# Kernel tuning notes

Hardware: AMD Instinct MI355X
Metric: run time of the kernel (lower is better)

The kernel has to match this reference:

```python
import math
import jax, jax.numpy as jnp
import numpy as np

_INIT_LOG_GAIN = math.log(5.0)
B, L, D = 4, 1024, 256


def setup_inputs() -> dict:
    key = jax.random.key(0)
    kq, kk = jax.random.split(key)
    q = jax.random.normal(kq, (B, L, D), dtype=jnp.float32)
    k = jax.random.normal(kk, (B, L, D), dtype=jnp.float32)
    P_prev = jnp.zeros((B, D, D), dtype=jnp.float32)
    log_gain = jnp.full((D,), _INIT_LOG_GAIN, dtype=jnp.float32)
    output_scale = jnp.ones((D,), dtype=jnp.float32)
    return {"q": q, "k": k, "P_prev": P_prev, "log_gain": log_gain,
            "output_scale": output_scale}


def reference(q, k, P_prev, log_gain, output_scale):
    """Sequential rank-1 projection-state update + normalized matvec + gated tanh.

    q, k: [B, L, D]; P_prev: [B, D, D]. Returns (q_out [B,L,D], P_final [B,D,D]).
    """
    gain = jnp.exp(log_gain)  # effective gain, [D]

    def step(P, qk_t):
        q_t, k_t = qk_t                                   # each [B, D]
        P = P + jnp.einsum('bi,bj->bij', k_t, k_t)        # rank-1 update
        fro = jnp.sqrt(jnp.sum(P * P, axis=(-2, -1), keepdims=True))
        P_norm = P / (fro + 1e-7)
        q_aligned = jnp.einsum('bij,bj->bi', P_norm, q_t)
        q_safe = jnp.tanh(gain * q_aligned) * output_scale
        return P, q_safe

    # scan over the L time axis
    P_final, outs = jax.lax.scan(step, P_prev,
                                 (jnp.swapaxes(q, 0, 1), jnp.swapaxes(k, 0, 1)))
    q_out = jnp.swapaxes(outs, 0, 1)  # [B, L, D]
    return q_out, P_final
```

## Files before the change

### kernel.cpp

```cpp
#include <hip/hip_runtime.h>
#include <math.h>


#define LDSPAD 68

typedef __attribute__((ext_vector_type(8))) short bf16x8;
typedef __attribute__((ext_vector_type(4))) float f32x4;

__device__ __forceinline__ unsigned short f2bf(float x) {
    union { float f; unsigned u; } c; c.f = x;
    return (unsigned short)((c.u + (0x7fffu + ((c.u >> 16) & 1u))) >> 16);
}
__device__ __forceinline__ unsigned f2bf2(float a, float b) {
    union { float f; unsigned u; } ca, cb; ca.f = a; cb.f = b;
    unsigned ua = ca.u + (0x7fffu + ((ca.u >> 16) & 1u));
    unsigned ub = cb.u + (0x7fffu + ((cb.u >> 16) & 1u));
    return (ua >> 16) | (ub & 0xffff0000u);
}
__device__ __forceinline__ void gload16(const void* g, const void* l) {
    __builtin_amdgcn_global_load_lds(
        (const __attribute__((address_space(1))) unsigned int*)g,
        (__attribute__((address_space(3))) unsigned int*)l, 16, 0, 0);
}
__device__ __forceinline__ bf16x8 ldsfrag(const unsigned short* lds, int row0, int g0, int lane) {
    int r = row0 + (lane & 15);
    int g = g0 + (lane >> 4);
    return *(const bf16x8*)(lds + r * 64 + (((g ^ (r & 7)) & 7) << 3));
}
__device__ __forceinline__ bf16x8 ldsfragf32(const char* tile, int row0, int lane) {
    int r = row0 + (lane & 15);
    int g0 = (lane >> 4) << 1;
    float4 a = *(const float4*)(tile + r * 128 + (((g0 ^ (r & 7)) & 7) << 4));
    float4 b = *(const float4*)(tile + r * 128 + ((((g0 + 1) ^ (r & 7)) & 7) << 4));
    union { unsigned u[4]; bf16x8 v; } o;
    o.u[0] = f2bf2(a.x, a.y); o.u[1] = f2bf2(a.z, a.w);
    o.u[2] = f2bf2(b.x, b.y); o.u[3] = f2bf2(b.z, b.w);
    return o.v;
}
#define MFMA16(a, b, c) __builtin_amdgcn_mfma_f32_16x16x32_bf16(a, b, c, 0, 0, 0)

__global__ __launch_bounds__(256) void k_gsp(
    const float* __restrict__ Q, const float* __restrict__ K,
    const float* __restrict__ Pprev,
    unsigned short* __restrict__ Sc, float* __restrict__ r2d, float* __restrict__ P4,
    unsigned short* __restrict__ KT, float* __restrict__ basePart,
    int B_, int L, int D, int nT, int nPairs)
{
    __shared__ char smem[49152];
    int tid = threadIdx.x, lane = tid & 63, w = tid >> 6;
    int fr = lane & 15, fq = lane >> 4;
    int nDt = D >> 6, nLt = L >> 6;
    int nGS = B_ * nPairs;
    int nP4 = B_ * nDt * nDt * 4;
    int nKT = B_ * nLt * nDt;
    int bx = blockIdx.x;
    int id = (bx < nGS) ? ((bx & 7) * (nGS >> 3) + (bx >> 3)) : bx;

    if (id < nGS) {
        int p = id % nPairs;
        int b = id / nPairs;
        int ti = (int)((sqrtf(8.f * p + 1.f) - 1.f) * 0.5f);
        while ((ti + 1) * (ti + 2) / 2 <= p) ti++;
        while (ti * (ti + 1) / 2 > p) ti--;
        int sj = p - ti * (ti + 1) / 2;

        const float* Qf = Q + (size_t)b * L * D;
        const float* Kf = K + (size_t)b * L * D;
        int t0 = ti * 64, s0 = sj * 64;
        int wr = w >> 1, wc = w & 1;

        f32x4 g00 = {0,0,0,0}, g01 = {0,0,0,0}, g10 = {0,0,0,0}, g11 = {0,0,0,0};
        f32x4 s00 = {0,0,0,0}, s01 = {0,0,0,0}, s10 = {0,0,0,0}, s11 = {0,0,0,0};

        auto STAGE = [&](int ck, int bo) {
            const float* Kt = Kf + (size_t)t0 * D + ck * 32;
            const float* Qt = Qf + (size_t)t0 * D + ck * 32;
            const float* Ks = Kf + (size_t)s0 * D + ck * 32;
            for (int c = w; c < 8; c += 4) {
                int lrow = c * 8 + (lane >> 3);
                int gof = lrow * D + ((((lane & 7) ^ (lrow & 7)) & 7) << 2);
                gload16(Kt + gof, smem + bo + c * 1024);
                gload16(Qt + gof, smem + bo + 8192 + c * 1024);
                gload16(Ks + gof, smem + bo + 16384 + c * 1024);
            }
        };

        STAGE(0, 0);
        __syncthreads();
        for (int ck = 0; ck < 8; ck++) {
            int cur = (ck & 1) * 24576;
            if (ck < 7) STAGE(ck + 1, 24576 - cur);
            const char* Kt = smem + cur;
            const char* Qt = Kt + 8192;
            const char* Ks = Kt + 16384;
            bf16x8 bK0 = ldsfragf32(Ks, wc * 32, lane);
            bf16x8 bK1 = ldsfragf32(Ks, wc * 32 + 16, lane);
            bf16x8 aK0 = ldsfragf32(Kt, wr * 32, lane);
            bf16x8 aK1 = ldsfragf32(Kt, wr * 32 + 16, lane);
            bf16x8 aQ0 = ldsfragf32(Qt, wr * 32, lane);
            bf16x8 aQ1 = ldsfragf32(Qt, wr * 32 + 16, lane);
            g00 = MFMA16(aK0, bK0, g00);
            g01 = MFMA16(aK0, bK1, g01);
            g10 = MFMA16(aK1, bK0, g10);
            g11 = MFMA16(aK1, bK1, g11);
            s00 = MFMA16(aQ0, bK0, s00);
            s01 = MFMA16(aQ0, bK1, s01);
            s10 = MFMA16(aQ1, bK0, s10);
            s11 = MFMA16(aQ1, bK1, s11);
            __syncthreads();
        }

        float rsv[2][4] = {{0, 0, 0, 0}, {0, 0, 0, 0}};
        unsigned short* sb = (unsigned short*)smem;
#define EPI(MI, NI, AG, AS) { _Pragma("unroll") \
        for (int reg = 0; reg < 4; reg++) { \
            int tl = wr * 32 + MI * 16 + fq * 4 + reg; \
            int sl2 = wc * 32 + NI * 16 + fr; \
            int t = ti * 64 + tl, s = sj * 64 + sl2; \
            float g = AG[reg]; \
            float wgt = (s < t) ? 2.f : (s == t ? 1.f : 0.f); \
            rsv[MI][reg] += wgt * g * g; \
            sb[tl * 64 + sl2] = f2bf((s <= t) ? AS[reg] : 0.f); \
        } }
        EPI(0, 0, g00, s00) EPI(0, 1, g01, s01)
        EPI(1, 0, g10, s10) EPI(1, 1, g11, s11)
#undef EPI
        __syncthreads();
        {
            unsigned short* ScT = Sc + ((size_t)(b * nPairs + p) << 12);
            const uint4* s4 = (const uint4*)sb;
            uint4* d4 = (uint4*)ScT;
            d4[tid] = s4[tid];
            d4[tid + 256] = s4[tid + 256];
        }
#pragma unroll
        for (int off = 1; off < 16; off <<= 1) {
#pragma unroll
            for (int mi = 0; mi < 2; mi++)
#pragma unroll
                for (int reg = 0; reg < 4; reg++)
                    rsv[mi][reg] += __shfl_xor(rsv[mi][reg], off);
        }
        if (fr == 0) {
#pragma unroll
            for (int mi = 0; mi < 2; mi++)
#pragma unroll
                for (int reg = 0; reg < 4; reg++) {
                    int t = ti * 64 + wr * 32 + mi * 16 + fq * 4 + reg;
                    r2d[((size_t)(b * 2 * nT) + sj * 2 + wc) * L + t] = rsv[mi][reg];
                }
        }
    } else if (id < nGS + nP4) {
        int id2 = id - nGS;
        int nIJ = nDt * nDt;
        int lc = id2 & 3;
        int ij = (id2 >> 2) % nIJ;
        int b = id2 / (4 * nIJ);
        int ib = (ij / nDt) * 64, jb = (ij % nDt) * 64;
        int tchunk = L >> 2;
        int tstart = lc * tchunk;
        const float* Kf = K + (size_t)b * L * D;
        float* lA = (float*)smem;
        float* lB = lA + 32 * LDSPAD;
        int tx = tid & 15, ty = tid >> 4;
        float acc[4][4] = {};
        for (int tc = 0; tc < tchunk; tc += 32) {
            __syncthreads();
            for (int f = tid; f < 512; f += 256) {
                int r = f >> 4, c4 = (f & 15) * 4;
                *(float4*)&lA[r * LDSPAD + c4] =
                    *(const float4*)(Kf + (size_t)(tstart + tc + r) * D + ib + c4);
                *(float4*)&lB[r * LDSPAD + c4] =
                    *(const float4*)(Kf + (size_t)(tstart + tc + r) * D + jb + c4);
            }
            __syncthreads();
#pragma unroll 8
            for (int t2 = 0; t2 < 32; t2++) {
                float4 av = *(const float4*)&lA[t2 * LDSPAD + ty * 4];
                float4 bv = *(const float4*)&lB[t2 * LDSPAD + tx * 4];
                float aa[4] = {av.x, av.y, av.z, av.w};
                float ba[4] = {bv.x, bv.y, bv.z, bv.w};
#pragma unroll
                for (int i = 0; i < 4; i++)
#pragma unroll
                    for (int j = 0; j < 4; j++) acc[i][j] += aa[i] * ba[j];
            }
        }
        float* dst = P4 + ((((size_t)b * nIJ + ij) * 4 + lc) * 4096);
#pragma unroll
        for (int i = 0; i < 4; i++) {
            float4 o = {acc[i][0], acc[i][1], acc[i][2], acc[i][3]};
            *(float4*)(dst + (ty * 4 + i) * 64 + tx * 4) = o;
        }
    } else if (id < nGS + nP4 + nKT) {
        int id2 = id - nGS - nP4;
        int dt = id2 % nDt, lt = (id2 / nDt) % nLt, b = id2 / (nDt * nLt);
        int l0 = lt * 64, d0 = dt * 64;
        const float* Kf = K + (size_t)b * L * D;
        unsigned short* KTp = KT + (size_t)b * D * L;
        float* lds = (float*)smem;
        int r = tid >> 2, cq = (tid & 3) << 4;
#pragma unroll
        for (int i = 0; i < 16; i += 4) {
            float4 kv = *(const float4*)(Kf + (size_t)(l0 + r) * D + d0 + cq + i);
            lds[r * 65 + cq + i] = kv.x;     lds[r * 65 + cq + i + 1] = kv.y;
            lds[r * 65 + cq + i + 2] = kv.z; lds[r * 65 + cq + i + 3] = kv.w;
        }
        __syncthreads();
        int d2 = tid >> 2, cl = (tid & 3) << 4;
#pragma unroll
        for (int i = 0; i < 16; i += 2) {
            *(unsigned*)(KTp + (size_t)(d0 + d2) * L + l0 + cl + i) =
                f2bf2(lds[(cl + i) * 65 + d2], lds[(cl + i + 1) * 65 + d2]);
        }
    } else {
        int id2 = id - nGS - nP4 - nKT;
        int n = D * D / 16;
        const float* P = Pprev + (size_t)(id2 >> 4) * D * D + (size_t)(id2 & 15) * n;
        float* lds = (float*)smem;
        float s = 0.f;
        for (int i = tid * 4; i < n; i += 1024) {
            float4 vv = *(const float4*)(P + i);
            s += vv.x * vv.x + vv.y * vv.y + vv.z * vv.z + vv.w * vv.w;
        }
#pragma unroll
        for (int off = 32; off; off >>= 1) s += __shfl_down(s, off);
        if (lane == 0) lds[w] = s;
        __syncthreads();
        if (tid == 0) basePart[id2] = lds[0] + lds[1] + lds[2] + lds[3];
    }
}

__global__ __launch_bounds__(256) void k_yp(
    const float* __restrict__ Q, const float* __restrict__ K,
    const float* __restrict__ Pprev, const float* __restrict__ log_gain,
    const float* __restrict__ oscale,
    const unsigned short* __restrict__ Sc, const float* __restrict__ r2d,
    const unsigned short* __restrict__ KT, const float* __restrict__ basePart,
    const float* __restrict__ P4,
    float* __restrict__ out, float* __restrict__ outP,
    int B_, int L, int D, int nT, int nPairs)
{
    __shared__ unsigned short ys[18432];
    __shared__ float invf[1024];
    __shared__ float wred[4];
    int tid = threadIdx.x, lane = tid & 63, w = tid >> 6;
    int fr = lane & 15, fq = lane >> 4;
    int nDt = D >> 6;
    int nDh = 16;
    int nY = B_ * (nT >> 1) * nDh;
    int bx = blockIdx.x;
    int id = (bx < nY) ? ((bx & 7) * (nY >> 3) + (bx >> 3)) : bx;

    if (id < nY) {
        int dh = id % nDh;
        int u = (id / nDh) % (nT >> 1);
        int b = id / (nDh * (nT >> 1));
        int d0 = dh * 16;

        float bb = 0.f;
#pragma unroll
        for (int i = 0; i < 16; i++) bb += basePart[b * 16 + i];

        int t0v = tid * 4;
        int ns = 2 * ((t0v >> 6) + 1);
        float4 vs = {0.f, 0.f, 0.f, 0.f};
        for (int j = 0; j < ns; j++) {
            float4 rr = *(const float4*)&r2d[((size_t)(b * 2 * nT) + j) * L + t0v];
            vs.x += rr.x; vs.y += rr.y; vs.z += rr.z; vs.w += rr.w;
        }
        float v[4] = {vs.x, vs.y, vs.z, vs.w};
        if (bb != 0.f) {
#pragma unroll
            for (int u2 = 0; u2 < 4; u2++) {
                int t = t0v + u2;
                const float* kt = K + ((size_t)b * L + t) * D;
                const float* P = Pprev + (size_t)b * D * D;
                float c = 0.f;
                for (int i = 0; i < D; i++) {
                    float a2 = 0.f;
                    for (int j2 = 0; j2 < D; j2++) a2 += P[i * D + j2] * kt[j2];
                    c += kt[i] * a2;
                }
                v[u2] += 2.f * c;
            }
        }
        v[1] += v[0]; v[2] += v[1]; v[3] += v[2];
        float tot = v[3], sc2 = tot;
        for (int off = 1; off < 64; off <<= 1) {
            float n2 = __shfl_up(sc2, off);
            if (lane >= off) sc2 += n2;
        }
        if (lane == 63) wred[w] = sc2;
        __syncthreads();
        float woff = 0.f;
        for (int i2 = 0; i2 < w; i2++) woff += wred[i2];
        float exc = woff + sc2 - tot;
#pragma unroll
        for (int u2 = 0; u2 < 4; u2++)
            invf[t0v + u2] = 1.f / (sqrtf(bb + exc + v[u2]) + 1e-7f);
        __syncthreads();

        int twl = w << 4;
        int ti0 = u, ti1 = nT - 1 - u;
        int pb0 = ti0 * (ti0 + 1) / 2, pb1 = ti1 * (ti1 + 1) / 2;
        const unsigned short* ScB = Sc + ((size_t)b * nPairs << 12);
        const unsigned short* KTb = KT + (size_t)b * D * L;

        f32x4 c0 = {0, 0, 0, 0};
        f32x4 c1 = {0, 0, 0, 0};

        auto STAGE = [&](int sj, int bo) {
            const unsigned short* T1p = ScB + ((size_t)(pb1 + sj) << 12);
            if (sj <= u) {
                const unsigned short* T0p = ScB + ((size_t)(pb0 + sj) << 12);
                for (int c = w; c < 8; c += 4) {
                    int lrow = c * 8 + (lane >> 3);
                    int go = lrow * 64 + ((((lane & 7) ^ (lrow & 7)) & 7) << 3);
                    gload16(T0p + go, ys + bo + c * 512);
                }
            }
            for (int c = w; c < 8; c += 4) {
                int lrow = c * 8 + (lane >> 3);
                int go = lrow * 64 + ((((lane & 7) ^ (lrow & 7)) & 7) << 3);
                gload16(T1p + go, ys + bo + 4096 + c * 512);
            }
            if (w < 2) {
                int lrow = w * 8 + (lane >> 3);
                int gsw = (((lane & 7) ^ (lrow & 7)) & 7) << 3;
                gload16(KTb + (size_t)(d0 + lrow) * L + sj * 64 + gsw,
                        ys + bo + 8192 + w * 512);
            }
        };

        STAGE(0, 0);
        __syncthreads();
        for (int sj = 0; sj <= ti1; sj++) {
            int cur = (sj & 1) * 9216;
            if (sj < ti1) STAGE(sj + 1, 9216 - cur);
            const unsigned short* S0 = ys + cur;
            const unsigned short* S1 = S0 + 4096;
            const unsigned short* KTl = S0 + 8192;
#pragma unroll
            for (int kc = 0; kc < 2; kc++) {
                bf16x8 b0 = ldsfrag(KTl, 0, kc * 4, lane);
                bf16x8 A1 = ldsfrag(S1, twl, kc * 4, lane);
                c1 = MFMA16(A1, b0, c1);
                if (sj <= ti0) {
                    bf16x8 A0 = ldsfrag(S0, twl, kc * 4, lane);
                    c0 = MFMA16(A0, b0, c0);
                }
            }
            __syncthreads();
        }

        if (bb != 0.f) {
            const float* Qf = Q + (size_t)b * L * D;
            const float* Pb = Pprev + (size_t)b * D * D;
            for (int jj = 0; jj < D; jj++) {
                float p0 = Pb[(size_t)(d0 + fr) * D + jj];
#pragma unroll
                for (int reg = 0; reg < 4; reg++) {
                    float q0v = Qf[(size_t)(ti0 * 64 + twl + fq * 4 + reg) * D + jj];
                    float q1v = Qf[(size_t)(ti1 * 64 + twl + fq * 4 + reg) * D + jj];
                    c0[reg] += q0v * p0;
                    c1[reg] += q1v * p0;
                }
            }
        }

        float gg0 = expf(log_gain[d0 + fr]), os0 = oscale[d0 + fr];
        float* outb = out + (size_t)b * L * D;
#pragma unroll
        for (int reg = 0; reg < 4; reg++) {
            int t0 = ti0 * 64 + twl + fq * 4 + reg;
            int t1 = ti1 * 64 + twl + fq * 4 + reg;
            outb[(size_t)t0 * D + d0 + fr] = tanhf(gg0 * c0[reg] * invf[t0]) * os0;
            outb[(size_t)t1 * D + d0 + fr] = tanhf(gg0 * c1[reg] * invf[t1]) * os0;
        }
    } else {
        int id2 = id - nY;
        int nIJ = nDt * nDt;
        size_t e = ((size_t)id2 * 256 + tid) * 8;
        int b = (int)(e / ((size_t)D * D));
        int rem = (int)(e % ((size_t)D * D));
        int i = rem / D, j = rem % D;
        int ij = (i >> 6) * nDt + (j >> 6);
        int li = i & 63, lj = j & 63;
        const float* src = P4 + ((size_t)b * nIJ + ij) * 4 * 4096 + li * 64 + lj;
        float4 o0 = *(const float4*)(Pprev + e);
        float4 o1 = *(const float4*)(Pprev + e + 4);
#pragma unroll
        for (int lc = 0; lc < 4; lc++) {
            float4 a0 = *(const float4*)(src + lc * 4096);
            float4 a1 = *(const float4*)(src + lc * 4096 + 4);
            o0.x += a0.x; o0.y += a0.y; o0.z += a0.z; o0.w += a0.w;
            o1.x += a1.x; o1.y += a1.y; o1.z += a1.z; o1.w += a1.w;
        }
        *(float4*)(outP + e) = o0;
        *(float4*)(outP + e + 4) = o1;
    }
}

extern "C" void kernel_launch(void* const* d_in, const int* in_sizes, int n_in,
                              void* d_out, int out_size, void* d_ws, size_t ws_size,
                              hipStream_t stream) {
    const float* q = (const float*)d_in[0];
    const float* k = (const float*)d_in[1];
    const float* Pprev = (const float*)d_in[2];
    const float* log_gain = (const float*)d_in[3];
    const float* oscale = (const float*)d_in[4];

    int D = in_sizes[3];
    int B = in_sizes[2] / (D * D);
    int L = in_sizes[0] / (B * D);
    int nT = L / 64;
    int nPairs = nT * (nT + 1) / 2;
    int nDt = D >> 6;
    int nLt = L >> 6;
    int nIJ = nDt * nDt;

    if (D != 256 || L != 1024) return;

    float* out = (float*)d_out;
    float* outP = out + (size_t)B * L * D;

    size_t sR = (size_t)B * L * 2 * nT;
    size_t sBP = 64;
    size_t sP4 = (size_t)B * nIJ * 4 * 4096;
    size_t sSc = (size_t)B * nPairs * 4096;
    size_t sKT = (size_t)B * D * L;
    size_t need = (sR + sBP + sP4) * sizeof(float) + (sSc + sKT) * 2;
    if (ws_size < need) return;

    float* r2d = (float*)d_ws;
    float* basePart = r2d + sR;
    float* P4 = basePart + sBP;
    unsigned short* Sc = (unsigned short*)(P4 + sP4);
    unsigned short* KT = Sc + sSc;

    int grid1 = B * nPairs + B * nIJ * 4 + B * nLt * nDt + B * 16;
    int grid2 = B * (nT >> 1) * 16 + (B * D * D) / 2048;

    k_gsp<<<grid1, 256, 0, stream>>>(q, k, Pprev, Sc, r2d, P4, KT, basePart,
                                     B, L, D, nT, nPairs);
    k_yp<<<grid2, 256, 0, stream>>>(q, k, Pprev, log_gain, oscale, Sc, r2d, KT,
                                    basePart, P4, out, outP, B, L, D, nT, nPairs);
}
```

Before: 56.62 us.

## Compute final P via split-bf16 MFMA and hoist per-batch norm scan to own kernel

The final-state rank-update K^T K, previously done with FP32 scalar FMA into four partial buffers and reduced in the second kernel, is now computed in the second kernel with bf16 MFMA using a hi/lo split of K (three products) for near-fp32 accuracy. The first kernel writes both high and low bf16 transposed K. The cumulative Frobenius-norm prefix scan, previously recomputed by every output block, moves into a small separate per-batch kernel that writes inverse norms. This trades an extra launch and the hi/lo storage traffic for less redundant work and tensor-core use.

```diff
diff --git a/kernel.cpp b/kernel.cpp
--- a/kernel.cpp
+++ b/kernel.cpp
@@ -1,8 +1,6 @@
 #include <hip/hip_runtime.h>
 #include <math.h>
 
-
-#define LDSPAD 68
 
 typedef __attribute__((ext_vector_type(8))) short bf16x8;
 typedef __attribute__((ext_vector_type(4))) float f32x4;
@@ -16,6 +14,9 @@
     unsigned ua = ca.u + (0x7fffu + ((ca.u >> 16) & 1u));
     unsigned ub = cb.u + (0x7fffu + ((cb.u >> 16) & 1u));
     return (ua >> 16) | (ub & 0xffff0000u);
+}
+__device__ __forceinline__ float bf2f(unsigned short h) {
+    union { unsigned u; float f; } c; c.u = ((unsigned)h) << 16; return c.f;
 }
 __device__ __forceinline__ void gload16(const void* g, const void* l) {
     __builtin_amdgcn_global_load_lds(
@@ -42,8 +43,9 @@
 __global__ __launch_bounds__(256) void k_gsp(
     const float* __restrict__ Q, const float* __restrict__ K,
     const float* __restrict__ Pprev,
-    unsigned short* __restrict__ Sc, float* __restrict__ r2d, float* __restrict__ P4,
-    unsigned short* __restrict__ KT, float* __restrict__ basePart,
+    unsigned short* __restrict__ Sc, float* __restrict__ r2d,
+    unsigned short* __restrict__ KThi, unsigned short* __restrict__ KTlo,
+    float* __restrict__ basePart,
     int B_, int L, int D, int nT, int nPairs)
 {
     __shared__ char smem[49152];
@@ -51,7 +53,6 @@
     int fr = lane & 15, fq = lane >> 4;
     int nDt = D >> 6, nLt = L >> 6;
     int nGS = B_ * nPairs;
-    int nP4 = B_ * nDt * nDt * 4;
     int nKT = B_ * nLt * nDt;
     int bx = blockIdx.x;
     int id = (bx < nGS) ? ((bx & 7) * (nGS >> 3) + (bx >> 3)) : bx;
@@ -150,54 +151,13 @@
                     r2d[((size_t)(b * 2 * nT) + sj * 2 + wc) * L + t] = rsv[mi][reg];
                 }
         }
-    } else if (id < nGS + nP4) {
+    } else if (id < nGS + nKT) {
         int id2 = id - nGS;
-        int nIJ = nDt * nDt;
-        int lc = id2 & 3;
-        int ij = (id2 >> 2) % nIJ;
-        int b = id2 / (4 * nIJ);
-        int ib = (ij / nDt) * 64, jb = (ij % nDt) * 64;
-        int tchunk = L >> 2;
-        int tstart = lc * tchunk;
-        const float* Kf = K + (size_t)b * L * D;
-        float* lA = (float*)smem;
-        float* lB = lA + 32 * LDSPAD;
-        int tx = tid & 15, ty = tid >> 4;
-        float acc[4][4] = {};
-        for (int tc = 0; tc < tchunk; tc += 32) {
-            __syncthreads();
-            for (int f = tid; f < 512; f += 256) {
-                int r = f >> 4, c4 = (f & 15) * 4;
-                *(float4*)&lA[r * LDSPAD + c4] =
-                    *(const float4*)(Kf + (size_t)(tstart + tc + r) * D + ib + c4);
-                *(float4*)&lB[r * LDSPAD + c4] =
-                    *(const float4*)(Kf + (size_t)(tstart + tc + r) * D + jb + c4);
-            }
-            __syncthreads();
-#pragma unroll 8
-            for (int t2 = 0; t2 < 32; t2++) {
-                float4 av = *(const float4*)&lA[t2 * LDSPAD + ty * 4];
-                float4 bv = *(const float4*)&lB[t2 * LDSPAD + tx * 4];
-                float aa[4] = {av.x, av.y, av.z, av.w};
-                float ba[4] = {bv.x, bv.y, bv.z, bv.w};
-#pragma unroll
-                for (int i = 0; i < 4; i++)
-#pragma unroll
-                    for (int j = 0; j < 4; j++) acc[i][j] += aa[i] * ba[j];
-            }
-        }
-        float* dst = P4 + ((((size_t)b * nIJ + ij) * 4 + lc) * 4096);
-#pragma unroll
-        for (int i = 0; i < 4; i++) {
-            float4 o = {acc[i][0], acc[i][1], acc[i][2], acc[i][3]};
-            *(float4*)(dst + (ty * 4 + i) * 64 + tx * 4) = o;
-        }
-    } else if (id < nGS + nP4 + nKT) {
-        int id2 = id - nGS - nP4;
         int dt = id2 % nDt, lt = (id2 / nDt) % nLt, b = id2 / (nDt * nLt);
         int l0 = lt * 64, d0 = dt * 64;
         const float* Kf = K + (size_t)b * L * D;
-        unsigned short* KTp = KT + (size_t)b * D * L;
+        unsigned short* KThp = KThi + (size_t)b * D * L;
+        unsigned short* KTlp = KTlo + (size_t)b * D * L;
         float* lds = (float*)smem;
         int r = tid >> 2, cq = (tid & 3) << 4;
 #pragma unroll
@@ -210,11 +170,15 @@
         int d2 = tid >> 2, cl = (tid & 3) << 4;
 #pragma unroll
         for (int i = 0; i < 16; i += 2) {
-            *(unsigned*)(KTp + (size_t)(d0 + d2) * L + l0 + cl + i) =
-                f2bf2(lds[(cl + i) * 65 + d2], lds[(cl + i + 1) * 65 + d2]);
+            float v0 = lds[(cl + i) * 65 + d2];
+            float v1 = lds[(cl + i + 1) * 65 + d2];
+            unsigned short h0 = f2bf(v0), h1 = f2bf(v1);
+            size_t off = (size_t)(d0 + d2) * L + l0 + cl + i;
+            *(unsigned*)(KThp + off) = (unsigned)h0 | ((unsigned)h1 << 16);
+            *(unsigned*)(KTlp + off) = f2bf2(v0 - bf2f(h0), v1 - bf2f(h1));
         }
     } else {
-        int id2 = id - nGS - nP4 - nKT;
+        int id2 = id - nGS - nKT;
         int n = D * D / 16;
         const float* P = Pprev + (size_t)(id2 >> 4) * D * D + (size_t)(id2 & 15) * n;
         float* lds = (float*)smem;
@@ -231,22 +195,71 @@
     }
 }
 
+__global__ __launch_bounds__(256) void k_scan(
+    const float* __restrict__ K, const float* __restrict__ Pprev,
+    const float* __restrict__ r2d, const float* __restrict__ basePart,
+    float* __restrict__ invfro, int B_, int L, int D, int nT)
+{
+    __shared__ float wred[4];
+    int b = blockIdx.x;
+    int tid = threadIdx.x, lane = tid & 63, w = tid >> 6;
+    float bb = 0.f;
+#pragma unroll
+    for (int i = 0; i < 16; i++) bb += basePart[b * 16 + i];
+
+    int t0v = tid * 4;
+    int ns = 2 * ((t0v >> 6) + 1);
+    float4 vs = {0.f, 0.f, 0.f, 0.f};
+    for (int j = 0; j < ns; j++) {
+        float4 rr = *(const float4*)&r2d[((size_t)(b * 2 * nT) + j) * L + t0v];
+        vs.x += rr.x; vs.y += rr.y; vs.z += rr.z; vs.w += rr.w;
+    }
+    float v[4] = {vs.x, vs.y, vs.z, vs.w};
+    if (bb != 0.f) {
+#pragma unroll
+        for (int u2 = 0; u2 < 4; u2++) {
+            int t = t0v + u2;
+            const float* kt = K + ((size_t)b * L + t) * D;
+            const float* P = Pprev + (size_t)b * D * D;
+            float c = 0.f;
+            for (int i = 0; i < D; i++) {
+                float a2 = 0.f;
+                for (int j2 = 0; j2 < D; j2++) a2 += P[i * D + j2] * kt[j2];
+                c += kt[i] * a2;
+            }
+            v[u2] += 2.f * c;
+        }
+    }
+    v[1] += v[0]; v[2] += v[1]; v[3] += v[2];
+    float tot = v[3], sc2 = tot;
+    for (int off = 1; off < 64; off <<= 1) {
+        float n2 = __shfl_up(sc2, off);
+        if (lane >= off) sc2 += n2;
+    }
+    if (lane == 63) wred[w] = sc2;
+    __syncthreads();
+    float woff = 0.f;
+    for (int i2 = 0; i2 < w; i2++) woff += wred[i2];
+    float exc = woff + sc2 - tot;
+#pragma unroll
+    for (int u2 = 0; u2 < 4; u2++)
+        invfro[(size_t)b * L + t0v + u2] = 1.f / (sqrtf(bb + exc + v[u2]) + 1e-7f);
+}
+
 __global__ __launch_bounds__(256) void k_yp(
-    const float* __restrict__ Q, const float* __restrict__ K,
+    const float* __restrict__ Q,
     const float* __restrict__ Pprev, const float* __restrict__ log_gain,
     const float* __restrict__ oscale,
-    const unsigned short* __restrict__ Sc, const float* __restrict__ r2d,
-    const unsigned short* __restrict__ KT, const float* __restrict__ basePart,
-    const float* __restrict__ P4,
+    const unsigned short* __restrict__ Sc, const float* __restrict__ invfro,
+    const unsigned short* __restrict__ KThi, const unsigned short* __restrict__ KTlo,
+    const float* __restrict__ basePart,
     float* __restrict__ out, float* __restrict__ outP,
     int B_, int L, int D, int nT, int nPairs)
 {
     __shared__ unsigned short ys[18432];
     __shared__ float invf[1024];
-    __shared__ float wred[4];
     int tid = threadIdx.x, lane = tid & 63, w = tid >> 6;
     int fr = lane & 15, fq = lane >> 4;
-    int nDt = D >> 6;
     int nDh = 16;
     int nY = B_ * (nT >> 1) * nDh;
     int bx = blockIdx.x;
@@ -261,51 +274,14 @@
         float bb = 0.f;
 #pragma unroll
         for (int i = 0; i < 16; i++) bb += basePart[b * 16 + i];
-
-        int t0v = tid * 4;
-        int ns = 2 * ((t0v >> 6) + 1);
-        float4 vs = {0.f, 0.f, 0.f, 0.f};
-        for (int j = 0; j < ns; j++) {
-            float4 rr = *(const float4*)&r2d[((size_t)(b * 2 * nT) + j) * L + t0v];
-            vs.x += rr.x; vs.y += rr.y; vs.z += rr.z; vs.w += rr.w;
-        }
-        float v[4] = {vs.x, vs.y, vs.z, vs.w};
-        if (bb != 0.f) {
-#pragma unroll
-            for (int u2 = 0; u2 < 4; u2++) {
-                int t = t0v + u2;
-                const float* kt = K + ((size_t)b * L + t) * D;
-                const float* P = Pprev + (size_t)b * D * D;
-                float c = 0.f;
-                for (int i = 0; i < D; i++) {
-                    float a2 = 0.f;
-                    for (int j2 = 0; j2 < D; j2++) a2 += P[i * D + j2] * kt[j2];
-                    c += kt[i] * a2;
-                }
-                v[u2] += 2.f * c;
-            }
-        }
-        v[1] += v[0]; v[2] += v[1]; v[3] += v[2];
-        float tot = v[3], sc2 = tot;
-        for (int off = 1; off < 64; off <<= 1) {
-            float n2 = __shfl_up(sc2, off);
-            if (lane >= off) sc2 += n2;
-        }
-        if (lane == 63) wred[w] = sc2;
-        __syncthreads();
-        float woff = 0.f;
-        for (int i2 = 0; i2 < w; i2++) woff += wred[i2];
-        float exc = woff + sc2 - tot;
-#pragma unroll
-        for (int u2 = 0; u2 < 4; u2++)
-            invf[t0v + u2] = 1.f / (sqrtf(bb + exc + v[u2]) + 1e-7f);
+        *(float4*)&invf[tid * 4] = *(const float4*)&invfro[(size_t)b * L + tid * 4];
         __syncthreads();
 
         int twl = w << 4;
         int ti0 = u, ti1 = nT - 1 - u;
         int pb0 = ti0 * (ti0 + 1) / 2, pb1 = ti1 * (ti1 + 1) / 2;
         const unsigned short* ScB = Sc + ((size_t)b * nPairs << 12);
-        const unsigned short* KTb = KT + (size_t)b * D * L;
+        const unsigned short* KTb = KThi + (size_t)b * D * L;
 
         f32x4 c0 = {0, 0, 0, 0};
         f32x4 c1 = {0, 0, 0, 0};
@@ -380,25 +356,54 @@
         }
     } else {
         int id2 = id - nY;
-        int nIJ = nDt * nDt;
-        size_t e = ((size_t)id2 * 256 + tid) * 8;
-        int b = (int)(e / ((size_t)D * D));
-        int rem = (int)(e % ((size_t)D * D));
-        int i = rem / D, j = rem % D;
-        int ij = (i >> 6) * nDt + (j >> 6);
-        int li = i & 63, lj = j & 63;
-        const float* src = P4 + ((size_t)b * nIJ + ij) * 4 * 4096 + li * 64 + lj;
-        float4 o0 = *(const float4*)(Pprev + e);
-        float4 o1 = *(const float4*)(Pprev + e + 4);
-#pragma unroll
-        for (int lc = 0; lc < 4; lc++) {
-            float4 a0 = *(const float4*)(src + lc * 4096);
-            float4 a1 = *(const float4*)(src + lc * 4096 + 4);
-            o0.x += a0.x; o0.y += a0.y; o0.z += a0.z; o0.w += a0.w;
-            o1.x += a1.x; o1.y += a1.y; o1.z += a1.z; o1.w += a1.w;
-        }
-        *(float4*)(outP + e) = o0;
-        *(float4*)(outP + e + 4) = o1;
+        int b = id2 >> 4, ij = id2 & 15;
+        int i0 = (ij >> 2) << 6, j0 = (ij & 3) << 6;
+        const unsigned short* Hb = KThi + (size_t)b * D * L;
+        const unsigned short* Lb = KTlo + (size_t)b * D * L;
+        int wr = w >> 1, wc = w & 1;
+        unsigned short* Ah = ys;
+        unsigned short* Al = ys + 4096;
+        unsigned short* Bh = ys + 8192;
+        unsigned short* Bl = ys + 12288;
+
+        f32x4 c00 = {0,0,0,0}, c01 = {0,0,0,0}, c10 = {0,0,0,0}, c11 = {0,0,0,0};
+        for (int ck = 0; ck < 16; ck++) {
+            __syncthreads();
+            for (int c = w; c < 8; c += 4) {
+                int lrow = c * 8 + (lane >> 3);
+                int gof = (((lane & 7) ^ (lrow & 7)) & 7) << 3;
+                gload16(Hb + (size_t)(i0 + lrow) * L + ck * 64 + gof, Ah + c * 512);
+                gload16(Lb + (size_t)(i0 + lrow) * L + ck * 64 + gof, Al + c * 512);
+                gload16(Hb + (size_t)(j0 + lrow) * L + ck * 64 + gof, Bh + c * 512);
+                gload16(Lb + (size_t)(j0 + lrow) * L + ck * 64 + gof, Bl + c * 512);
+            }
+            __syncthreads();
+#pragma unroll
+            for (int kc = 0; kc < 2; kc++) {
+                bf16x8 ah0 = ldsfrag(Ah, wr * 32, kc * 4, lane);
+                bf16x8 ah1 = ldsfrag(Ah, wr * 32 + 16, kc * 4, lane);
+                bf16x8 al0 = ldsfrag(Al, wr * 32, kc * 4, lane);
+                bf16x8 al1 = ldsfrag(Al, wr * 32 + 16, kc * 4, lane);
+                bf16x8 bh0 = ldsfrag(Bh, wc * 32, kc * 4, lane);
+                bf16x8 bh1 = ldsfrag(Bh, wc * 32 + 16, kc * 4, lane);
+                bf16x8 bl0 = ldsfrag(Bl, wc * 32, kc * 4, lane);
+                bf16x8 bl1 = ldsfrag(Bl, wc * 32 + 16, kc * 4, lane);
+                c00 = MFMA16(ah0, bh0, c00); c00 = MFMA16(ah0, bl0, c00); c00 = MFMA16(al0, bh0, c00);
+                c01 = MFMA16(ah0, bh1, c01); c01 = MFMA16(ah0, bl1, c01); c01 = MFMA16(al0, bh1, c01);
+                c10 = MFMA16(ah1, bh0, c10); c10 = MFMA16(ah1, bl0, c10); c10 = MFMA16(al1, bh0, c10);
+                c11 = MFMA16(ah1, bh1, c11); c11 = MFMA16(ah1, bl1, c11); c11 = MFMA16(al1, bh1, c11);
+            }
+        }
+        const float* Pb = Pprev + (size_t)b * D * D;
+        float* Ob = outP + (size_t)b * D * D;
+#define PEPI(MI, NI, ACC) { _Pragma("unroll") \
+        for (int reg = 0; reg < 4; reg++) { \
+            int i = i0 + wr * 32 + MI * 16 + fq * 4 + reg; \
+            int j = j0 + wc * 32 + NI * 16 + fr; \
+            Ob[(size_t)i * D + j] = Pb[(size_t)i * D + j] + ACC[reg]; \
+        } }
+        PEPI(0, 0, c00) PEPI(0, 1, c01) PEPI(1, 0, c10) PEPI(1, 1, c11)
+#undef PEPI
     }
 }
 
@@ -418,7 +423,6 @@
     int nPairs = nT * (nT + 1) / 2;
     int nDt = D >> 6;
     int nLt = L >> 6;
-    int nIJ = nDt * nDt;
 
     if (D != 256 || L != 1024) return;
 
@@ -427,23 +431,25 @@
 
     size_t sR = (size_t)B * L * 2 * nT;
     size_t sBP = 64;
-    size_t sP4 = (size_t)B * nIJ * 4 * 4096;
+    size_t sI = (size_t)B * L;
     size_t sSc = (size_t)B * nPairs * 4096;
     size_t sKT = (size_t)B * D * L;
-    size_t need = (sR + sBP + sP4) * sizeof(float) + (sSc + sKT) * 2;
+    size_t need = (sR + sBP + sI) * sizeof(float) + (sSc + 2 * sKT) * 2;
     if (ws_size < need) return;
 
     float* r2d = (float*)d_ws;
     float* basePart = r2d + sR;
-    float* P4 = basePart + sBP;
-    unsigned short* Sc = (unsigned short*)(P4 + sP4);
-    unsigned short* KT = Sc + sSc;
-
-    int grid1 = B * nPairs + B * nIJ * 4 + B * nLt * nDt + B * 16;
-    int grid2 = B * (nT >> 1) * 16 + (B * D * D) / 2048;
-
-    k_gsp<<<grid1, 256, 0, stream>>>(q, k, Pprev, Sc, r2d, P4, KT, basePart,
+    float* invfro = basePart + sBP;
+    unsigned short* Sc = (unsigned short*)(invfro + sI);
+    unsigned short* KThi = Sc + sSc;
+    unsigned short* KTlo = KThi + sKT;
+
+    int grid1 = B * nPairs + B * nLt * nDt + B * 16;
+    int grid2 = B * (nT >> 1) * 16 + B * nDt * nDt;
+
+    k_gsp<<<grid1, 256, 0, stream>>>(q, k, Pprev, Sc, r2d, KThi, KTlo, basePart,
                                      B, L, D, nT, nPairs);
-    k_yp<<<grid2, 256, 0, stream>>>(q, k, Pprev, log_gain, oscale, Sc, r2d, KT,
-                                    basePart, P4, out, outP, B, L, D, nT, nPairs);
-}
+    k_scan<<<B, 256, 0, stream>>>(k, Pprev, r2d, basePart, invfro, B, L, D, nT);
+    k_yp<<<grid2, 256, 0, stream>>>(q, Pprev, log_gain, oscale, Sc, invfro, KThi, KTlo,
+                                    basePart, out, outP, B, L, D, nT, nPairs);
+}
```

Result: faster. 50.16 us (-11.4%).
